# Optimization experiments

Measured on AMD Instinct MI355X. Metric: run time of the kernel, lower is better.

Reference implementation:

```python
import jax, jax.numpy as jnp
import numpy as np

HIDDEN = 1280
HEADS = 16
HEAD_DIM = HIDDEN // HEADS  # 80
B, N = 2, 2048


def _rotate_half(x):
    half = x.shape[-1] // 2
    return jnp.concatenate([-x[..., half:], x[..., :half]], axis=-1)


def setup_inputs() -> dict:
    key = jax.random.key(0)
    ks = jax.random.split(key, 7)
    x = jax.random.normal(ks[0], (B, N, HIDDEN), dtype=jnp.float32)
    cos = jax.random.uniform(ks[1], (N, HEAD_DIM), dtype=jnp.float32)
    sin = jax.random.uniform(ks[2], (N, HEAD_DIM), dtype=jnp.float32)
    s = 1.0 / np.sqrt(HIDDEN)
    qkv_w = jax.random.normal(ks[3], (HIDDEN, 3 * HIDDEN), dtype=jnp.float32) * s
    qkv_b = jax.random.normal(ks[4], (3 * HIDDEN,), dtype=jnp.float32) * 0.02
    proj_w = jax.random.normal(ks[5], (HIDDEN, HIDDEN), dtype=jnp.float32) * s
    proj_b = jax.random.normal(ks[6], (HIDDEN,), dtype=jnp.float32) * 0.02
    return {"x": x, "cos": cos, "sin": sin, "qkv_w": qkv_w, "qkv_b": qkv_b,
            "proj_w": proj_w, "proj_b": proj_b}


def reference(x, cos, sin, qkv_w, qkv_b, proj_w, proj_b):
    b, n, _ = x.shape
    scale = 1.0 / np.sqrt(HEAD_DIM).astype(np.float32)
    # fused QKV projection
    qkv = x @ qkv_w + qkv_b                                # [b, n, 3*hidden]
    qkv = qkv.reshape(b, n, 3, HEADS, HEAD_DIM)
    qkv = jnp.transpose(qkv, (2, 0, 3, 1, 4))              # [3, b, h, n, hd]
    q, k, v = qkv[0], qkv[1], qkv[2]
    # 2D RoPE
    cos_b = cos[None, None, :, :]
    sin_b = sin[None, None, :, :]
    q = q * cos_b + _rotate_half(q) * sin_b
    k = k * cos_b + _rotate_half(k) * sin_b
    # manual softmax attention
    scores = jnp.einsum('bhqd,bhkd->bhqk', q, k) * scale   # [b, h, n, n]
    attn = jax.nn.softmax(scores, axis=-1)
    out = jnp.einsum('bhqk,bhkd->bhqd', attn, v)           # [b, h, n, hd]
    out = jnp.transpose(out, (0, 2, 1, 3)).reshape(b, n, HIDDEN)
    return out @ proj_w + proj_b
```

## Files before the change

### kernel.cpp

```cpp
#include <hip/hip_runtime.h>
#include <hip/hip_bf16.h>
#include <math.h>

#define HIDDEN 1280
#define HEADS 16
#define HD 80
#define HALF 40
#define BB 2
#define NN 2048
#define MROWS (BB * NN)
#define QSCALE ((float)(0.11180339887498949 * 1.4426950408889634))

typedef __attribute__((ext_vector_type(8))) _Float16 f16x8;
typedef __attribute__((ext_vector_type(4))) float f32x4;

#define AS1 __attribute__((address_space(1)))
#define AS3 __attribute__((address_space(3)))

__device__ __forceinline__ void splitf16(float x, ushort& hi, ushort& lo) {
    _Float16 h = (_Float16)x;
    _Float16 l = (_Float16)(x - (float)h);
    hi = __builtin_bit_cast(ushort, h);
    lo = __builtin_bit_cast(ushort, l);
}

__device__ __forceinline__ ushort f2h(float x) {
    _Float16 h = (_Float16)x;
    return __builtin_bit_cast(ushort, h);
}

__global__ __launch_bounds__(256) void split_f16_kernel(
    const float* __restrict__ in, ushort* __restrict__ hi,
    ushort* __restrict__ lo, int n4)
{
    int i = blockIdx.x * 256 + threadIdx.x;
    if (i >= n4) return;
    float4 v = ((const float4*)in)[i];
    ushort4 h, l;
    splitf16(v.x, h.x, l.x);
    splitf16(v.y, h.y, l.y);
    splitf16(v.z, h.z, l.z);
    splitf16(v.w, h.w, l.w);
    ((ushort4*)hi)[i] = h;
    ((ushort4*)lo)[i] = l;
}

__global__ __launch_bounds__(256) void tsplit_f16_kernel(
    const float* __restrict__ W, ushort* __restrict__ T, int K, int N)
{
    __shared__ float s[32][33];
    const int n0 = blockIdx.x * 32;
    const int k0 = blockIdx.y * 32;
    {
        int tn = threadIdx.x & 31, tk = threadIdx.x >> 5;
        #pragma unroll
        for (int i = 0; i < 4; ++i)
            s[tk + i * 8][tn] = W[(size_t)(k0 + tk + i * 8) * N + n0 + tn];
    }
    __syncthreads();
    {
        int tk = threadIdx.x & 31, tn = threadIdx.x >> 5;
        #pragma unroll
        for (int i = 0; i < 4; ++i)
            T[(size_t)(n0 + tn + i * 8) * K + k0 + tk] = f2h(s[tk][tn + i * 8]);
    }
}

#define BM 128
#define BN 128
#define BK 32

__global__ __launch_bounds__(256) void gemm_f16x2_kernel(
    const ushort* __restrict__ Ahi, const ushort* __restrict__ Alo,
    const ushort* __restrict__ Bh,
    const float* __restrict__ bias, float* __restrict__ C,
    int M, int N, int K)
{
    __shared__ __align__(16) ushort lds[3 * 128 * 32];

    const int tid = threadIdx.x;
    const int wid = tid >> 6;
    const int lane = tid & 63;
    const int col0 = blockIdx.x * BN;
    const int row0 = blockIdx.y * BM;
    const int wy = wid >> 1, wx = wid & 1;
    const int lrow = lane >> 2;
    const int lchunk = lane & 3;

    f32x4 acc[4][4] = {};

    for (int k0 = 0; k0 < K; k0 += BK) {
        __syncthreads();
        #pragma unroll
        for (int i = 0; i < 6; ++i) {
            int s = wid + i * 4;
            int tile = s >> 3, t = s & 7;
            const ushort* src = (tile == 0) ? Ahi : (tile == 1) ? Alo : Bh;
            int srow = (tile < 2) ? row0 : col0;
            const ushort* g = src + (size_t)(srow + t * 16 + lrow) * K + k0 + lchunk * 8;
            ushort* l = lds + tile * 4096 + t * 512 + lane * 8;
            __builtin_amdgcn_global_load_lds(
                (const AS1 unsigned int*)g, (AS3 unsigned int*)l, 16, 0, 0);
        }
        __syncthreads();

        const int q = lane >> 4;
        const int r = lane & 15;
        f16x8 ah[4], al[4], bf[4];
        #pragma unroll
        for (int i = 0; i < 4; ++i) {
            int arow = wy * 64 + i * 16 + r;
            ah[i] = *(const f16x8*)(lds + 0 * 4096 + arow * 32 + q * 8);
            al[i] = *(const f16x8*)(lds + 1 * 4096 + arow * 32 + q * 8);
            int brow = wx * 64 + i * 16 + r;
            bf[i] = *(const f16x8*)(lds + 2 * 4096 + brow * 32 + q * 8);
        }
        #pragma unroll
        for (int i = 0; i < 4; ++i) {
            #pragma unroll
            for (int j = 0; j < 4; ++j) {
                acc[i][j] = __builtin_amdgcn_mfma_f32_16x16x32_f16(al[i], bf[j], acc[i][j], 0, 0, 0);
                acc[i][j] = __builtin_amdgcn_mfma_f32_16x16x32_f16(ah[i], bf[j], acc[i][j], 0, 0, 0);
            }
        }
    }

    const int q = lane >> 4, r = lane & 15;
    #pragma unroll
    for (int i = 0; i < 4; ++i) {
        #pragma unroll
        for (int j = 0; j < 4; ++j) {
            int col = col0 + wx * 64 + j * 16 + r;
            float b = bias[col];
            #pragma unroll
            for (int v = 0; v < 4; ++v) {
                int row = row0 + wy * 64 + i * 16 + q * 4 + v;
                C[(size_t)row * N + col] = acc[i][j][v] + b;
            }
        }
    }
}

__global__ __launch_bounds__(512, 2) void gemm_f16x2_256_kernel(
    const ushort* __restrict__ Ahi, const ushort* __restrict__ Alo,
    const ushort* __restrict__ Bh,
    const float* __restrict__ bias, float* __restrict__ C,
    int M, int N, int K, int nbx)
{
    __shared__ __align__(16) ushort lds[3 * 3 * 8192];

    const int tid = threadIdx.x;
    const int wid = tid >> 6;
    const int lane = tid & 63;
    const int q = lane >> 4, r = lane & 15;
    const int wr = wid >> 2, wc = wid & 3;

    int id = blockIdx.x;
    {
        int nwg = gridDim.x;
        if ((nwg & 7) == 0) {
            int c = nwg >> 3;
            id = (id & 7) * c + (id >> 3);
        }
    }
    const int row0 = (id / nbx) * 256;
    const int col0 = (id % nbx) * 256;

    const ushort* gsrc[6];
    int ldst[6];
    #pragma unroll
    for (int j = 0; j < 6; ++j) {
        int pj = j >> 1;
        int rloc = wid * 32 + (j & 1) * 16 + (lane >> 2);
        int sl = (lane & 3) ^ ((rloc >> 1) & 3);
        const ushort* base = (pj == 0) ? Ahi : (pj == 1) ? Alo : Bh;
        int grow = ((pj < 2) ? row0 : col0) + rloc;
        gsrc[j] = base + (size_t)grow * K + sl * 8;
        ldst[j] = pj * 8192 + (wid * 32 + (j & 1) * 16) * 32 + lane * 8;
    }

    const int NT = K / 32;

    #pragma unroll
    for (int j = 0; j < 6; ++j)
        __builtin_amdgcn_global_load_lds((const AS1 unsigned int*)(gsrc[j]),
            (AS3 unsigned int*)(lds + ldst[j]), 16, 0, 0);
    #pragma unroll
    for (int j = 0; j < 6; ++j)
        __builtin_amdgcn_global_load_lds((const AS1 unsigned int*)(gsrc[j] + 32),
            (AS3 unsigned int*)(lds + 24576 + ldst[j]), 16, 0, 0);
    asm volatile("s_waitcnt vmcnt(6)" ::: "memory");
    __builtin_amdgcn_s_barrier();

    const int soff = (q ^ ((r >> 1) & 3)) * 8;
    const int arow0 = wr * 128 + r;
    const int brow0 = wc * 64 + r;

    f32x4 acc[8][4] = {};
    f16x8 ah[4], al[4], bf[4];

    int cb = 0;
    int nb = 49152;

    for (int t = 0; t < NT; ++t) {
        const ushort* A0 = lds + cb;
        const ushort* A1 = lds + cb + 8192;
        const ushort* Bp = lds + cb + 16384;
        ushort* nbuf = lds + nb;
        const bool st = (t + 2 < NT);
        const int ko = (t + 2) * 32;

        #pragma unroll
        for (int m = 0; m < 4; ++m) {
            int ro = (arow0 + m * 16) * 32 + soff;
            ah[m] = *(const f16x8*)(A0 + ro);
            al[m] = *(const f16x8*)(A1 + ro);
        }
        #pragma unroll
        for (int n = 0; n < 2; ++n)
            bf[n] = *(const f16x8*)(Bp + (brow0 + n * 16) * 32 + soff);
        if (st) {
            __builtin_amdgcn_global_load_lds((const AS1 unsigned int*)(gsrc[0] + ko),
                (AS3 unsigned int*)(nbuf + ldst[0]), 16, 0, 0);
            __builtin_amdgcn_global_load_lds((const AS1 unsigned int*)(gsrc[1] + ko),
                (AS3 unsigned int*)(nbuf + ldst[1]), 16, 0, 0);
        }
        __builtin_amdgcn_s_barrier();
        asm volatile("s_waitcnt lgkmcnt(0)" ::: "memory");
        __builtin_amdgcn_sched_barrier(0);
        __builtin_amdgcn_s_setprio(1);
        #pragma unroll
        for (int m = 0; m < 4; ++m) {
            #pragma unroll
            for (int n = 0; n < 2; ++n) {
                acc[m][n] = __builtin_amdgcn_mfma_f32_16x16x32_f16(al[m], bf[n], acc[m][n], 0, 0, 0);
                acc[m][n] = __builtin_amdgcn_mfma_f32_16x16x32_f16(ah[m], bf[n], acc[m][n], 0, 0, 0);
            }
        }
        __builtin_amdgcn_s_setprio(0);
        __builtin_amdgcn_s_barrier();

        #pragma unroll
        for (int n = 2; n < 4; ++n)
            bf[n] = *(const f16x8*)(Bp + (brow0 + n * 16) * 32 + soff);
        if (st) {
            __builtin_amdgcn_global_load_lds((const AS1 unsigned int*)(gsrc[2] + ko),
                (AS3 unsigned int*)(nbuf + ldst[2]), 16, 0, 0);
            __builtin_amdgcn_global_load_lds((const AS1 unsigned int*)(gsrc[3] + ko),
                (AS3 unsigned int*)(nbuf + ldst[3]), 16, 0, 0);
        }
        __builtin_amdgcn_s_barrier();
        asm volatile("s_waitcnt lgkmcnt(0)" ::: "memory");
        __builtin_amdgcn_sched_barrier(0);
        __builtin_amdgcn_s_setprio(1);
        #pragma unroll
        for (int m = 0; m < 4; ++m) {
            #pragma unroll
            for (int n = 2; n < 4; ++n) {
                acc[m][n] = __builtin_amdgcn_mfma_f32_16x16x32_f16(al[m], bf[n], acc[m][n], 0, 0, 0);
                acc[m][n] = __builtin_amdgcn_mfma_f32_16x16x32_f16(ah[m], bf[n], acc[m][n], 0, 0, 0);
            }
        }
        __builtin_amdgcn_s_setprio(0);
        __builtin_amdgcn_s_barrier();

        #pragma unroll
        for (int m = 0; m < 4; ++m) {
            int ro = (arow0 + (m + 4) * 16) * 32 + soff;
            ah[m] = *(const f16x8*)(A0 + ro);
            al[m] = *(const f16x8*)(A1 + ro);
        }
        if (st) {
            __builtin_amdgcn_global_load_lds((const AS1 unsigned int*)(gsrc[4] + ko),
                (AS3 unsigned int*)(nbuf + ldst[4]), 16, 0, 0);
            __builtin_amdgcn_global_load_lds((const AS1 unsigned int*)(gsrc[5] + ko),
                (AS3 unsigned int*)(nbuf + ldst[5]), 16, 0, 0);
        }
        __builtin_amdgcn_s_barrier();
        asm volatile("s_waitcnt lgkmcnt(0)" ::: "memory");
        __builtin_amdgcn_sched_barrier(0);
        __builtin_amdgcn_s_setprio(1);
        #pragma unroll
        for (int m = 0; m < 4; ++m) {
            #pragma unroll
            for (int n = 2; n < 4; ++n) {
                acc[m + 4][n] = __builtin_amdgcn_mfma_f32_16x16x32_f16(al[m], bf[n], acc[m + 4][n], 0, 0, 0);
                acc[m + 4][n] = __builtin_amdgcn_mfma_f32_16x16x32_f16(ah[m], bf[n], acc[m + 4][n], 0, 0, 0);
            }
        }
        __builtin_amdgcn_s_setprio(0);
        __builtin_amdgcn_s_barrier();

        __builtin_amdgcn_s_setprio(1);
        #pragma unroll
        for (int m = 0; m < 4; ++m) {
            #pragma unroll
            for (int n = 0; n < 2; ++n) {
                acc[m + 4][n] = __builtin_amdgcn_mfma_f32_16x16x32_f16(al[m], bf[n], acc[m + 4][n], 0, 0, 0);
                acc[m + 4][n] = __builtin_amdgcn_mfma_f32_16x16x32_f16(ah[m], bf[n], acc[m + 4][n], 0, 0, 0);
            }
        }
        __builtin_amdgcn_s_setprio(0);
        if (st)
            asm volatile("s_waitcnt vmcnt(6)" ::: "memory");
        else if (t + 1 < NT)
            asm volatile("s_waitcnt vmcnt(0)" ::: "memory");
        __builtin_amdgcn_s_barrier();

        cb += 24576; if (cb == 73728) cb = 0;
        nb += 24576; if (nb == 73728) nb = 0;
    }

    #pragma unroll
    for (int m = 0; m < 8; ++m) {
        #pragma unroll
        for (int n = 0; n < 4; ++n) {
            int col = col0 + wc * 64 + n * 16 + r;
            float b = bias[col];
            #pragma unroll
            for (int v = 0; v < 4; ++v) {
                int row = row0 + wr * 128 + m * 16 + q * 4 + v;
                C[(size_t)row * N + col] = acc[m][n][v] + b;
            }
        }
    }
}

__global__ __launch_bounds__(256) void rope_split_kernel(
    const float* __restrict__ qkv, const float* __restrict__ cos_t,
    const float* __restrict__ sin_t,
    ushort* __restrict__ qf, ushort* __restrict__ kf,
    ushort* __restrict__ vt)
{
    __shared__ float s_v[64][84];
    const int tid = threadIdx.x;
    const int b = blockIdx.z, h = blockIdx.y;
    const int n0 = blockIdx.x * 64;
    const int bh = b * HEADS + h;

    #pragma unroll
    for (int i = 0; i < 5; ++i) {
        int u = tid + i * 256;
        int n = u / 20, c = u % 20;
        const float* src = qkv + (size_t)(b * NN + n0 + n) * 3840 + 2 * HIDDEN + h * HD + c * 4;
        *(float4*)(&s_v[n][c * 4]) = *(const float4*)src;
    }

    for (int u = tid; u < 640; u += 256) {
        int n = u / 10, p = u % 10;
        int d = p * 4;
        int ng = n0 + n;
        size_t rowb = (size_t)(b * NN + ng) * 3840;
        float4 c0 = *(const float4*)(cos_t + ng * HD + d);
        float4 c1 = *(const float4*)(cos_t + ng * HD + d + HALF);
        float4 s0 = *(const float4*)(sin_t + ng * HD + d);
        float4 s1 = *(const float4*)(sin_t + ng * HD + d + HALF);
        size_t qo = ((size_t)bh * NN + ng) * 96;
        {
            float4 x0 = *(const float4*)(qkv + rowb + h * HD + d);
            float4 x1 = *(const float4*)(qkv + rowb + h * HD + d + HALF);
            ushort4 h4a, h4b;
            h4a.x = f2h((x0.x * c0.x - x1.x * s0.x) * QSCALE);
            h4a.y = f2h((x0.y * c0.y - x1.y * s0.y) * QSCALE);
            h4a.z = f2h((x0.z * c0.z - x1.z * s0.z) * QSCALE);
            h4a.w = f2h((x0.w * c0.w - x1.w * s0.w) * QSCALE);
            h4b.x = f2h((x1.x * c1.x + x0.x * s1.x) * QSCALE);
            h4b.y = f2h((x1.y * c1.y + x0.y * s1.y) * QSCALE);
            h4b.z = f2h((x1.z * c1.z + x0.z * s1.z) * QSCALE);
            h4b.w = f2h((x1.w * c1.w + x0.w * s1.w) * QSCALE);
            *(ushort4*)(qf + qo + d) = h4a;
            *(ushort4*)(qf + qo + d + HALF) = h4b;
        }
        {
            float4 x0 = *(const float4*)(qkv + rowb + HIDDEN + h * HD + d);
            float4 x1 = *(const float4*)(qkv + rowb + HIDDEN + h * HD + d + HALF);
            ushort4 h4a, h4b;
            h4a.x = f2h(x0.x * c0.x - x1.x * s0.x);
            h4a.y = f2h(x0.y * c0.y - x1.y * s0.y);
            h4a.z = f2h(x0.z * c0.z - x1.z * s0.z);
            h4a.w = f2h(x0.w * c0.w - x1.w * s0.w);
            h4b.x = f2h(x1.x * c1.x + x0.x * s1.x);
            h4b.y = f2h(x1.y * c1.y + x0.y * s1.y);
            h4b.z = f2h(x1.z * c1.z + x0.z * s1.z);
            h4b.w = f2h(x1.w * c1.w + x0.w * s1.w);
            *(ushort4*)(kf + qo + d) = h4a;
            *(ushort4*)(kf + qo + d + HALF) = h4b;
        }
    }

    {
        int which = tid >> 7;
        int u = tid & 127;
        int n = u >> 1, part = u & 1;
        size_t o = ((size_t)bh * NN + n0 + n) * 96 + 80 + part * 8;
        uint4 z = {0u, 0u, 0u, 0u};
        if (which == 0) *(uint4*)(qf + o) = z;
        else            *(uint4*)(kf + o) = z;
    }
    __syncthreads();

    for (int u = tid; u < 320; u += 256) {
        int d = u >> 2, nc = u & 3;
        ushort hs[16];
        #pragma unroll
        for (int kk = 0; kk < 16; ++kk)
            hs[kk] = f2h(s_v[nc * 16 + kk][d]);
        size_t o = ((size_t)bh * HD + d) * NN + n0 + nc * 16;
        uint4 w0, w1;
        w0.x = (uint)hs[0] | ((uint)hs[1] << 16);
        w0.y = (uint)hs[2] | ((uint)hs[3] << 16);
        w0.z = (uint)hs[4] | ((uint)hs[5] << 16);
        w0.w = (uint)hs[6] | ((uint)hs[7] << 16);
        w1.x = (uint)hs[8] | ((uint)hs[9] << 16);
        w1.y = (uint)hs[10] | ((uint)hs[11] << 16);
        w1.z = (uint)hs[12] | ((uint)hs[13] << 16);
        w1.w = (uint)hs[14] | ((uint)hs[15] << 16);
        *(uint4*)(vt + o) = w0;
        *(uint4*)(vt + o + 8) = w1;
    }
}

__global__ __launch_bounds__(256, 2) void attn_mfma_kernel(
    const ushort* __restrict__ qf, const ushort* __restrict__ kf,
    const ushort* __restrict__ vt,
    ushort* __restrict__ ao_hi, ushort* __restrict__ ao_lo)
{
    __shared__ __align__(16) ushort lds[34816];
    _Float16* p_s = (_Float16*)(lds + 26624);

    const int tid = threadIdx.x;
    const int wave = tid >> 6, lane = tid & 63;
    const int quad = lane >> 4, r = lane & 15;
    const int b = blockIdx.z, h = blockIdx.y;
    const int bh = b * HEADS + h;
    const int q0 = blockIdx.x * 128;

    const size_t kb = (size_t)bh * NN * 96;
    const size_t vb = (size_t)bh * HD * NN;

    const ushort* gptr[7];
    int ldso[7];
    #pragma unroll
    for (int i = 0; i < 7; ++i) {
        int s = wave + i * 4;
        if (s < 16) {
            int row = s * 4 + (lane >> 4);
            int t = lane & 15;
            int g = t ^ (row & 7);
            if (g >= 12) g = 0;
            gptr[i] = kf + kb + (size_t)row * 96 + g * 8;
            ldso[i] = s * 512 + lane * 8;
        } else if (s < 26) {
            int ts = s - 16;
            gptr[i] = vt + vb + (size_t)(ts * 8 + (lane >> 3)) * NN
                      + (size_t)(((lane & 7) ^ (lane >> 3)) * 8);
            ldso[i] = 8192 + ts * 512 + lane * 8;
        } else {
            gptr[i] = nullptr;
            ldso[i] = 0;
        }
    }

    f16x8 qfr[2][3];
    #pragma unroll
    for (int mt = 0; mt < 2; ++mt)
        #pragma unroll
        for (int c = 0; c < 3; ++c) {
            size_t o = ((size_t)bh * NN + q0 + wave * 32 + mt * 16 + r) * 96 + c * 32 + quad * 8;
            qfr[mt][c] = *(const f16x8*)(qf + o);
        }

    f32x4 oacc[2][5] = {};
    float l_part[2][4] = {};

    #pragma unroll
    for (int i = 0; i < 7; ++i) {
        int s = wave + i * 4;
        if (s < 26) {
            __builtin_amdgcn_global_load_lds((const AS1 unsigned int*)gptr[i],
                (AS3 unsigned int*)(lds + ldso[i]), 16, 0, 0);
            gptr[i] += (s < 16) ? 6144 : 64;
        }
    }
    asm volatile("s_waitcnt vmcnt(0)" ::: "memory");
    __builtin_amdgcn_s_barrier();

    int cur = 0;
    for (int j0 = 0; j0 < NN; j0 += 64) {
        const int nxt = 13312 - cur;
        if (j0 + 64 < NN) {
            #pragma unroll
            for (int i = 0; i < 7; ++i) {
                int s = wave + i * 4;
                if (s < 26) {
                    __builtin_amdgcn_global_load_lds((const AS1 unsigned int*)gptr[i],
                        (AS3 unsigned int*)(lds + nxt + ldso[i]), 16, 0, 0);
                    gptr[i] += (s < 16) ? 6144 : 64;
                }
            }
        }

        const ushort* k_s = lds + cur;
        const _Float16* v_s = (const _Float16*)(lds + cur + 8192);

        f32x4 sc[2][4] = {};
        __builtin_amdgcn_s_setprio(1);
        #pragma unroll
        for (int jt = 0; jt < 4; ++jt) {
            f16x8 kbf[3];
            int j = jt * 16 + r;
            #pragma unroll
            for (int c = 0; c < 3; ++c) {
                int ch = (c * 4 + quad) ^ (r & 7);
                kbf[c] = *(const f16x8*)(k_s + j * 128 + ch * 8);
            }
            #pragma unroll
            for (int mt = 0; mt < 2; ++mt)
                #pragma unroll
                for (int c = 0; c < 3; ++c)
                    sc[mt][jt] = __builtin_amdgcn_mfma_f32_16x16x32_f16(qfr[mt][c], kbf[c], sc[mt][jt], 0, 0, 0);
        }
        __builtin_amdgcn_s_setprio(0);

        #pragma unroll
        for (int mt = 0; mt < 2; ++mt) {
            #pragma unroll
            for (int v = 0; v < 4; ++v) {
                float ps = 0.0f;
                #pragma unroll
                for (int jt = 0; jt < 4; ++jt) {
                    float p = __builtin_amdgcn_exp2f(sc[mt][jt][v]);
                    sc[mt][jt][v] = p;
                    ps += p;
                }
                l_part[mt][v] += ps;
            }
            int rowbase = wave * 32 + mt * 16 + quad * 4;
            #pragma unroll
            for (int jt = 0; jt < 4; ++jt) {
                int bks = (jt * 2 + (r >> 3)) ^ (quad << 1);
                #pragma unroll
                for (int v = 0; v < 4; ++v)
                    p_s[(rowbase + v) * 64 + bks * 8 + (r & 7)] = (_Float16)sc[mt][jt][v];
            }
        }

        f16x8 pa[2][2];
        #pragma unroll
        for (int mt = 0; mt < 2; ++mt)
            #pragma unroll
            for (int cc = 0; cc < 2; ++cc) {
                int rowp = wave * 32 + mt * 16 + r;
                int bks = (cc * 4 + quad) ^ (((r >> 2) & 3) << 1);
                pa[mt][cc] = *(const f16x8*)(p_s + rowp * 64 + bks * 8);
            }

        __builtin_amdgcn_s_setprio(1);
        #pragma unroll
        for (int dt = 0; dt < 5; ++dt)
            #pragma unroll
            for (int cc = 0; cc < 2; ++cc) {
                int ck = (cc * 4 + quad) ^ (r & 7);
                f16x8 vbf = *(const f16x8*)(v_s + (dt * 16 + r) * 64 + ck * 8);
                oacc[0][dt] = __builtin_amdgcn_mfma_f32_16x16x32_f16(pa[0][cc], vbf, oacc[0][dt], 0, 0, 0);
                oacc[1][dt] = __builtin_amdgcn_mfma_f32_16x16x32_f16(pa[1][cc], vbf, oacc[1][dt], 0, 0, 0);
            }
        __builtin_amdgcn_s_setprio(0);

        asm volatile("s_waitcnt vmcnt(0)" ::: "memory");
        __builtin_amdgcn_s_barrier();
        cur = nxt;
    }

    float inv_l[2][4];
    #pragma unroll
    for (int mt = 0; mt < 2; ++mt)
        #pragma unroll
        for (int v = 0; v < 4; ++v) {
            float l = l_part[mt][v];
            l += __shfl_xor(l, 1);
            l += __shfl_xor(l, 2);
            l += __shfl_xor(l, 4);
            l += __shfl_xor(l, 8);
            inv_l[mt][v] = 1.0f / l;
        }

    __syncthreads();
    #pragma unroll
    for (int mt = 0; mt < 2; ++mt)
        #pragma unroll
        for (int v = 0; v < 4; ++v) {
            int row = wave * 32 + mt * 16 + quad * 4 + v;
            #pragma unroll
            for (int dt = 0; dt < 5; ++dt) {
                float o = oacc[mt][dt][v] * inv_l[mt][v];
                ushort hh, ll;
                splitf16(o, hh, ll);
                lds[row * 80 + dt * 16 + r] = hh;
                lds[10240 + row * 80 + dt * 16 + r] = ll;
            }
        }
    __syncthreads();
    {
        size_t gbase = ((size_t)b * NN + q0) * HIDDEN + h * HD;
        #pragma unroll
        for (int i = 0; i < 10; ++i) {
            int u = tid + i * 256;
            int plane = u / 1280, idx = u % 1280;
            int row = idx / 10, part = idx % 10;
            uint4 w = *(const uint4*)(lds + plane * 10240 + idx * 8);
            ushort* dst = (plane ? ao_lo : ao_hi) + gbase + (size_t)row * HIDDEN + part * 8;
            *(uint4*)dst = w;
        }
    }
}

extern "C" void kernel_launch(void* const* d_in, const int* in_sizes, int n_in,
                              void* d_out, int out_size, void* d_ws, size_t ws_size,
                              hipStream_t stream)
{
    const float* x      = (const float*)d_in[0];
    const float* cos_t  = (const float*)d_in[1];
    const float* sin_t  = (const float*)d_in[2];
    const float* qkv_w  = (const float*)d_in[3];
    const float* qkv_b  = (const float*)d_in[4];
    const float* proj_w = (const float*)d_in[5];
    const float* proj_b = (const float*)d_in[6];
    float* out = (float*)d_out;

    char* ws = (char*)d_ws;
    float*  qkv   = (float*)ws;
    ushort* ao_hi = (ushort*)ws;
    ushort* ao_lo = (ushort*)(ws + 10485760);
    ushort* wT    = (ushort*)(ws + 62914560);
    ushort* vt    = (ushort*)(ws + 62914560);
    ushort* a_hi  = (ushort*)(ws + 82575360);
    ushort* a_lo  = (ushort*)(ws + 93061120);
    ushort* q_f   = (ushort*)(ws + 83886080);
    ushort* k_f   = (ushort*)(ws + 96468992);

    split_f16_kernel<<<(MROWS * HIDDEN / 4 + 255) / 256, 256, 0, stream>>>(
        x, a_hi, a_lo, MROWS * HIDDEN / 4);

    tsplit_f16_kernel<<<dim3(3 * HIDDEN / 32, HIDDEN / 32), 256, 0, stream>>>(
        qkv_w, wT, HIDDEN, 3 * HIDDEN);

    gemm_f16x2_256_kernel<<<dim3((MROWS / 256) * (3 * HIDDEN / 256)), 512, 0, stream>>>(
        a_hi, a_lo, wT, qkv_b, qkv, MROWS, 3 * HIDDEN, HIDDEN, 3 * HIDDEN / 256);

    rope_split_kernel<<<dim3(NN / 64, HEADS, BB), 256, 0, stream>>>(
        qkv, cos_t, sin_t, q_f, k_f, vt);

    attn_mfma_kernel<<<dim3(NN / 128, HEADS, BB), 256, 0, stream>>>(
        q_f, k_f, vt, ao_hi, ao_lo);

    tsplit_f16_kernel<<<dim3(HIDDEN / 32, HIDDEN / 32), 256, 0, stream>>>(
        proj_w, wT, HIDDEN, HIDDEN);

    gemm_f16x2_kernel<<<dim3(HIDDEN / BN, MROWS / BM), 256, 0, stream>>>(
        ao_hi, ao_lo, wT, proj_b, out, MROWS, HIDDEN, HIDDEN);
}
```

Before: 321.6 us.

## Split attention block across 8 waves with 16 query rows each

```diff
diff --git a/kernel.cpp b/kernel.cpp
--- a/kernel.cpp
+++ b/kernel.cpp
@@ -420,7 +420,7 @@
     }
 }
 
-__global__ __launch_bounds__(256, 2) void attn_mfma_kernel(
+__global__ __launch_bounds__(512, 4) void attn_mfma_kernel(
     const ushort* __restrict__ qf, const ushort* __restrict__ kf,
     const ushort* __restrict__ vt,
     ushort* __restrict__ ao_hi, ushort* __restrict__ ao_lo)
@@ -438,11 +438,11 @@
     const size_t kb = (size_t)bh * NN * 96;
     const size_t vb = (size_t)bh * HD * NN;
 
-    const ushort* gptr[7];
-    int ldso[7];
-    #pragma unroll
-    for (int i = 0; i < 7; ++i) {
-        int s = wave + i * 4;
+    const ushort* gptr[4];
+    int ldso[4];
+    #pragma unroll
+    for (int i = 0; i < 4; ++i) {
+        int s = wave + i * 8;
         if (s < 16) {
             int row = s * 4 + (lane >> 4);
             int t = lane & 15;
@@ -461,21 +461,19 @@
         }
     }
 
-    f16x8 qfr[2][3];
-    #pragma unroll
-    for (int mt = 0; mt < 2; ++mt)
-        #pragma unroll
-        for (int c = 0; c < 3; ++c) {
-            size_t o = ((size_t)bh * NN + q0 + wave * 32 + mt * 16 + r) * 96 + c * 32 + quad * 8;
-            qfr[mt][c] = *(const f16x8*)(qf + o);
-        }
-
-    f32x4 oacc[2][5] = {};
-    float l_part[2][4] = {};
-
-    #pragma unroll
-    for (int i = 0; i < 7; ++i) {
-        int s = wave + i * 4;
+    f16x8 qfr[3];
+    #pragma unroll
+    for (int c = 0; c < 3; ++c) {
+        size_t o = ((size_t)bh * NN + q0 + wave * 16 + r) * 96 + c * 32 + quad * 8;
+        qfr[c] = *(const f16x8*)(qf + o);
+    }
+
+    f32x4 oacc[5] = {};
+    float l_part[4] = {};
+
+    #pragma unroll
+    for (int i = 0; i < 4; ++i) {
+        int s = wave + i * 8;
         if (s < 26) {
             __builtin_amdgcn_global_load_lds((const AS1 unsigned int*)gptr[i],
                 (AS3 unsigned int*)(lds + ldso[i]), 16, 0, 0);
@@ -490,8 +488,8 @@
         const int nxt = 13312 - cur;
         if (j0 + 64 < NN) {
             #pragma unroll
-            for (int i = 0; i < 7; ++i) {
-                int s = wave + i * 4;
+            for (int i = 0; i < 4; ++i) {
+                int s = wave + i * 8;
                 if (s < 26) {
                     __builtin_amdgcn_global_load_lds((const AS1 unsigned int*)gptr[i],
                         (AS3 unsigned int*)(lds + nxt + ldso[i]), 16, 0, 0);
@@ -503,7 +501,7 @@
         const ushort* k_s = lds + cur;
         const _Float16* v_s = (const _Float16*)(lds + cur + 8192);
 
-        f32x4 sc[2][4] = {};
+        f32x4 sc[4] = {};
         __builtin_amdgcn_s_setprio(1);
         #pragma unroll
         for (int jt = 0; jt < 4; ++jt) {
@@ -515,45 +513,40 @@
                 kbf[c] = *(const f16x8*)(k_s + j * 128 + ch * 8);
             }
             #pragma unroll
-            for (int mt = 0; mt < 2; ++mt)
-                #pragma unroll
-                for (int c = 0; c < 3; ++c)
-                    sc[mt][jt] = __builtin_amdgcn_mfma_f32_16x16x32_f16(qfr[mt][c], kbf[c], sc[mt][jt], 0, 0, 0);
+            for (int c = 0; c < 3; ++c)
+                sc[jt] = __builtin_amdgcn_mfma_f32_16x16x32_f16(qfr[c], kbf[c], sc[jt], 0, 0, 0);
         }
         __builtin_amdgcn_s_setprio(0);
 
         #pragma unroll
-        for (int mt = 0; mt < 2; ++mt) {
-            #pragma unroll
-            for (int v = 0; v < 4; ++v) {
-                float ps = 0.0f;
-                #pragma unroll
-                for (int jt = 0; jt < 4; ++jt) {
-                    float p = __builtin_amdgcn_exp2f(sc[mt][jt][v]);
-                    sc[mt][jt][v] = p;
-                    ps += p;
-                }
-                l_part[mt][v] += ps;
-            }
-            int rowbase = wave * 32 + mt * 16 + quad * 4;
+        for (int v = 0; v < 4; ++v) {
+            float ps = 0.0f;
+            #pragma unroll
+            for (int jt = 0; jt < 4; ++jt) {
+                float p = __builtin_amdgcn_exp2f(sc[jt][v]);
+                sc[jt][v] = p;
+                ps += p;
+            }
+            l_part[v] += ps;
+        }
+        {
+            int rowbase = wave * 16 + quad * 4;
             #pragma unroll
             for (int jt = 0; jt < 4; ++jt) {
                 int bks = (jt * 2 + (r >> 3)) ^ (quad << 1);
                 #pragma unroll
                 for (int v = 0; v < 4; ++v)
-                    p_s[(rowbase + v) * 64 + bks * 8 + (r & 7)] = (_Float16)sc[mt][jt][v];
-            }
-        }
-
-        f16x8 pa[2][2];
-        #pragma unroll
-        for (int mt = 0; mt < 2; ++mt)
-            #pragma unroll
-            for (int cc = 0; cc < 2; ++cc) {
-                int rowp = wave * 32 + mt * 16 + r;
-                int bks = (cc * 4 + quad) ^ (((r >> 2) & 3) << 1);
-                pa[mt][cc] = *(const f16x8*)(p_s + rowp * 64 + bks * 8);
-            }
+                    p_s[(rowbase + v) * 64 + bks * 8 + (r & 7)] = (_Float16)sc[jt][v];
+            }
+        }
+
+        f16x8 pa[2];
+        #pragma unroll
+        for (int cc = 0; cc < 2; ++cc) {
+            int rowp = wave * 16 + r;
+            int bks = (cc * 4 + quad) ^ (((r >> 2) & 3) << 1);
+            pa[cc] = *(const f16x8*)(p_s + rowp * 64 + bks * 8);
+        }
 
         __builtin_amdgcn_s_setprio(1);
         #pragma unroll
@@ -562,8 +555,7 @@
             for (int cc = 0; cc < 2; ++cc) {
                 int ck = (cc * 4 + quad) ^ (r & 7);
                 f16x8 vbf = *(const f16x8*)(v_s + (dt * 16 + r) * 64 + ck * 8);
-                oacc[0][dt] = __builtin_amdgcn_mfma_f32_16x16x32_f16(pa[0][cc], vbf, oacc[0][dt], 0, 0, 0);
-                oacc[1][dt] = __builtin_amdgcn_mfma_f32_16x16x32_f16(pa[1][cc], vbf, oacc[1][dt], 0, 0, 0);
+                oacc[dt] = __builtin_amdgcn_mfma_f32_16x16x32_f16(pa[cc], vbf, oacc[dt], 0, 0, 0);
             }
         __builtin_amdgcn_s_setprio(0);
 
@@ -572,40 +564,36 @@
         cur = nxt;
     }
 
-    float inv_l[2][4];
-    #pragma unroll
-    for (int mt = 0; mt < 2; ++mt)
-        #pragma unroll
-        for (int v = 0; v < 4; ++v) {
-            float l = l_part[mt][v];
-            l += __shfl_xor(l, 1);
-            l += __shfl_xor(l, 2);
-            l += __shfl_xor(l, 4);
-            l += __shfl_xor(l, 8);
-            inv_l[mt][v] = 1.0f / l;
-        }
+    float inv_l[4];
+    #pragma unroll
+    for (int v = 0; v < 4; ++v) {
+        float l = l_part[v];
+        l += __shfl_xor(l, 1);
+        l += __shfl_xor(l, 2);
+        l += __shfl_xor(l, 4);
+        l += __shfl_xor(l, 8);
+        inv_l[v] = 1.0f / l;
+    }
 
     __syncthreads();
     #pragma unroll
-    for (int mt = 0; mt < 2; ++mt)
-        #pragma unroll
-        for (int v = 0; v < 4; ++v) {
-            int row = wave * 32 + mt * 16 + quad * 4 + v;
-            #pragma unroll
-            for (int dt = 0; dt < 5; ++dt) {
-                float o = oacc[mt][dt][v] * inv_l[mt][v];
-                ushort hh, ll;
-                splitf16(o, hh, ll);
-                lds[row * 80 + dt * 16 + r] = hh;
-                lds[10240 + row * 80 + dt * 16 + r] = ll;
-            }
-        }
+    for (int v = 0; v < 4; ++v) {
+        int row = wave * 16 + quad * 4 + v;
+        #pragma unroll
+        for (int dt = 0; dt < 5; ++dt) {
+            float o = oacc[dt][v] * inv_l[v];
+            ushort hh, ll;
+            splitf16(o, hh, ll);
+            lds[row * 80 + dt * 16 + r] = hh;
+            lds[10240 + row * 80 + dt * 16 + r] = ll;
+        }
+    }
     __syncthreads();
     {
         size_t gbase = ((size_t)b * NN + q0) * HIDDEN + h * HD;
         #pragma unroll
-        for (int i = 0; i < 10; ++i) {
-            int u = tid + i * 256;
+        for (int i = 0; i < 5; ++i) {
+            int u = tid + i * 512;
             int plane = u / 1280, idx = u % 1280;
             int row = idx / 10, part = idx % 10;
             uint4 w = *(const uint4*)(lds + plane * 10240 + idx * 8);
@@ -651,7 +639,7 @@
     rope_split_kernel<<<dim3(NN / 64, HEADS, BB), 256, 0, stream>>>(
         qkv, cos_t, sin_t, q_f, k_f, vt);
 
-    attn_mfma_kernel<<<dim3(NN / 128, HEADS, BB), 256, 0, stream>>>(
+    attn_mfma_kernel<<<dim3(NN / 128, HEADS, BB), 512, 0, stream>>>(
         q_f, k_f, vt, ao_hi, ao_lo);
 
     tsplit_f16_kernel<<<dim3(HIDDEN / 32, HIDDEN / 32), 256, 0, stream>>>(
```

Measured after the change: 318.1 us. No clear change (-1.1%).
